# Optimization experiments

Measured on AMD Instinct MI355X. Metric: run time of the kernel, lower is better.

## Reference

```python
import jax, jax.numpy as jnp
import numpy as np

N_HEADS = 16
ALIBI_BIAS_MAX = 8


def _alibi_bias(n_heads, seq_len):
    # MPT build_alibi_bias: bias[h, j] = -(seq_len-1-j) * slope_h, arranged [1,H,1,S]
    pos = jnp.arange(1 - seq_len, 1, dtype=jnp.float32).reshape(1, 1, 1, seq_len)
    m = jnp.arange(1, n_heads + 1, dtype=jnp.float32) * (ALIBI_BIAS_MAX / n_heads)
    slopes = (1.0 / jnp.exp2(m)).reshape(1, n_heads, 1, 1)
    return pos * slopes  # [1,H,1,S]


def setup_inputs() -> dict:
    key = jax.random.key(0)
    k1, k2, k3 = jax.random.split(key, 3)
    B, S, D = 1, 2048, 2048
    x = jax.random.normal(k1, (B, S, D), dtype=jnp.float32)
    # Wqkv: Linear(D, 3D, bias=False); out_proj: Linear(D, D, bias=False)
    w_qkv = jax.random.normal(k2, (3 * D, D), dtype=jnp.float32) * (1.0 / np.sqrt(D))
    w_out = jax.random.normal(k3, (D, D), dtype=jnp.float32) * (1.0 / np.sqrt(D))
    return {"x": x, "w_qkv": w_qkv, "w_out": w_out}


def reference(x, w_qkv, w_out):
    B, S, D = x.shape
    H = N_HEADS
    d = D // H
    qkv = x @ w_qkv.T                              # [B,S,3D]
    q, k, v = jnp.split(qkv, 3, axis=-1)
    q = q.reshape(B, S, H, d).transpose(0, 2, 1, 3)  # [B,H,S,d]
    k = k.reshape(B, S, H, d).transpose(0, 2, 1, 3)
    v = v.reshape(B, S, H, d).transpose(0, 2, 1, 3)
    scale = 1.0 / np.sqrt(d)
    scores = jnp.einsum('bhqd,bhkd->bhqk', q, k) * scale  # [B,H,S,S]
    scores = scores + _alibi_bias(H, S)
    min_val = jnp.finfo(scores.dtype).min
    causal = jnp.tril(jnp.ones((S, S), dtype=bool))
    scores = jnp.where(causal[None, None, :, :], scores, min_val)
    probs = jax.nn.softmax(scores.astype(jnp.float32), axis=-1).astype(q.dtype)
    out = jnp.einsum('bhqk,bhkd->bhqd', probs, v)  # [B,H,S,d]
    out = out.transpose(0, 2, 1, 3).reshape(B, S, D)
    return out @ w_out.T
```

## Files before the change

### kernel.cpp

```cpp
#include <hip/hip_runtime.h>

typedef __bf16 bf16;
typedef __bf16 bf16x8 __attribute__((ext_vector_type(8)));
typedef __bf16 bf16x4 __attribute__((ext_vector_type(4)));
typedef float f32x4 __attribute__((ext_vector_type(4)));

#if __has_builtin(__builtin_amdgcn_exp2f)
#define EXP2(x) __builtin_amdgcn_exp2f(x)
#else
#define EXP2(x) exp2f(x)
#endif

__device__ __forceinline__ void gload_lds16(const void* g, void* l) {
  __builtin_amdgcn_global_load_lds(
      (const __attribute__((address_space(1))) void*)g,
      (__attribute__((address_space(3))) void*)l, 16, 0, 0);
}

__global__ __launch_bounds__(256) void cast_all(const float* __restrict__ x,
                                                const float* __restrict__ wqkv,
                                                const float* __restrict__ wout,
                                                bf16* __restrict__ x_bf,
                                                bf16* __restrict__ wqkv_bf,
                                                bf16* __restrict__ wout_bf) {
  const int b = blockIdx.x;
  const float* src;
  bf16* dst;
  int i;
  if (b < 4096) {
    src = x; dst = x_bf; i = b * 1024 + threadIdx.x * 4;
  } else if (b < 16384) {
    src = wqkv; dst = wqkv_bf; i = (b - 4096) * 1024 + threadIdx.x * 4;
  } else {
    src = wout; dst = wout_bf; i = (b - 16384) * 1024 + threadIdx.x * 4;
  }
  float4 v = *(const float4*)(src + i);
  bf16x4 o = {(bf16)v.x, (bf16)v.y, (bf16)v.z, (bf16)v.w};
  *(bf16x4*)(dst + i) = o;
}

__global__ __launch_bounds__(256) void gemm1_qkv(const bf16* __restrict__ A,
                                                 const bf16* __restrict__ B,
                                                 bf16* __restrict__ qb,
                                                 bf16* __restrict__ kb,
                                                 bf16* __restrict__ vt) {
  constexpr int K = 2048;
  __shared__ bf16 As[128 * 32];
  __shared__ bf16 Bs[128 * 32];
  const int t = threadIdx.x;
  const int w = t >> 6, l = t & 63;
  const int lr = l & 15, lg = l >> 4;
  const int nwg = 768;
  int lin = blockIdx.y * 48 + blockIdx.x;
  lin = (lin & 7) * (nwg >> 3) + (lin >> 3);
  const int bn = lin % 48;
  const int bm = lin / 48;
  const int wr = w >> 1, wc = w & 1;

  f32x4 acc[4][4] = {};
  const int row0 = t >> 2;
  const int cc0 = (t & 3) * 8;

  for (int k0 = 0; k0 < K; k0 += 32) {
#pragma unroll
    for (int r = 0; r < 2; ++r) {
      const int row = r * 64 + row0;
      gload_lds16(A + (size_t)(bm * 128 + row) * K + k0 + cc0,
                  (char*)As + (r * 256 + w * 64) * 16);
      gload_lds16(B + (size_t)(bn * 128 + row) * K + k0 + cc0,
                  (char*)Bs + (r * 256 + w * 64) * 16);
    }
    __syncthreads();
    bf16x8 af[4], bfr[4];
#pragma unroll
    for (int i = 0; i < 4; ++i) {
      af[i] = *(const bf16x8*)((const char*)As + (wr * 64 + i * 16 + lr) * 64 + lg * 16);
      bfr[i] = *(const bf16x8*)((const char*)Bs + (wc * 64 + i * 16 + lr) * 64 + lg * 16);
    }
#pragma unroll
    for (int mi = 0; mi < 4; ++mi)
#pragma unroll
      for (int ni = 0; ni < 4; ++ni)
        acc[mi][ni] = __builtin_amdgcn_mfma_f32_16x16x32_bf16(af[mi], bfr[ni],
                                                              acc[mi][ni], 0, 0, 0);
    __syncthreads();
  }

  const int mb = bm * 128 + wr * 64 + lg * 4;
  const int nb = bn * 128 + wc * 64 + lr;
  if (bn * 128 < 4096) {
    bf16* dst = (bn * 128 < 2048) ? qb : kb;
#pragma unroll
    for (int mi = 0; mi < 4; ++mi) {
      const int mg = mb + mi * 16;
#pragma unroll
      for (int ni = 0; ni < 4; ++ni) {
        const int ng = (nb + ni * 16) & 2047;
#pragma unroll
        for (int rr = 0; rr < 4; ++rr)
          dst[(size_t)(mg + rr) * 2048 + ng] = (bf16)acc[mi][ni][rr];
      }
    }
  } else {
#pragma unroll
    for (int mi = 0; mi < 4; ++mi) {
      const int mg = mb + mi * 16;
#pragma unroll
      for (int ni = 0; ni < 4; ++ni) {
        const int dc = nb + ni * 16 - 4096;
        bf16x4 pk = {(bf16)acc[mi][ni][0], (bf16)acc[mi][ni][1],
                     (bf16)acc[mi][ni][2], (bf16)acc[mi][ni][3]};
        *(bf16x4*)(vt + (size_t)dc * 2048 + mg) = pk;
      }
    }
  }
}

__global__ __launch_bounds__(256) void gemm2_64x128(const bf16* __restrict__ A,
                                                    const bf16* __restrict__ B,
                                                    float* __restrict__ Cf) {
  constexpr int K = 2048, N = 2048;
  __shared__ bf16 As[64 * 32];
  __shared__ bf16 Bs[128 * 32];
  const int t = threadIdx.x;
  const int w = t >> 6, l = t & 63;
  const int lr = l & 15, lg = l >> 4;
  int lin = blockIdx.y * 16 + blockIdx.x;
  lin = (lin & 7) * 64 + (lin >> 3);
  const int bn = lin % 16;
  const int bm = lin / 16;

  f32x4 acc[4][2] = {};

  for (int k0 = 0; k0 < K; k0 += 32) {
    {
      const int row = t >> 2;
      gload_lds16(A + (size_t)(bm * 64 + row) * K + k0 + (t & 3) * 8,
                  (char*)As + (w * 64) * 16);
    }
#pragma unroll
    for (int r = 0; r < 2; ++r) {
      const int c = r * 256 + t;
      const int row = c >> 2;
      gload_lds16(B + (size_t)(bn * 128 + row) * K + k0 + (c & 3) * 8,
                  (char*)Bs + (r * 256 + w * 64) * 16);
    }
    __syncthreads();
    bf16x8 af[4], bfr[2];
#pragma unroll
    for (int i = 0; i < 4; ++i)
      af[i] = *(const bf16x8*)((const char*)As + (i * 16 + lr) * 64 + lg * 16);
#pragma unroll
    for (int i = 0; i < 2; ++i)
      bfr[i] = *(const bf16x8*)((const char*)Bs + (w * 32 + i * 16 + lr) * 64 + lg * 16);
#pragma unroll
    for (int mi = 0; mi < 4; ++mi)
#pragma unroll
      for (int ni = 0; ni < 2; ++ni)
        acc[mi][ni] = __builtin_amdgcn_mfma_f32_16x16x32_bf16(af[mi], bfr[ni],
                                                              acc[mi][ni], 0, 0, 0);
    __syncthreads();
  }

  const int mb = bm * 64 + lg * 4;
  const int nb = bn * 128 + w * 32 + lr;
#pragma unroll
  for (int mi = 0; mi < 4; ++mi) {
    const int mg = mb + mi * 16;
#pragma unroll
    for (int ni = 0; ni < 2; ++ni) {
      const int ng = nb + ni * 16;
#pragma unroll
      for (int rr = 0; rr < 4; ++rr)
        Cf[(size_t)(mg + rr) * N + ng] = acc[mi][ni][rr];
    }
  }
}

__global__ __launch_bounds__(256) void attn_kernel(const bf16* __restrict__ qb,
                                                   const bf16* __restrict__ kb,
                                                   const bf16* __restrict__ vt,
                                                   bf16* __restrict__ out) {
  constexpr int S = 2048, D = 2048;
  __shared__ bf16 Ks[2][64 * 128];
  __shared__ bf16 Vs[2][128 * 64];
  __shared__ bf16 Ps[4][16 * 64];
  const int t = threadIdx.x;
  const int w = t >> 6, l = t & 63;
  const int lr = l & 15, lg = l >> 4;
  const int b = blockIdx.x;
  const int h = b & 15;
  const int qt = (b < 256) ? (31 - (b >> 4)) : ((b - 256) >> 4);
  const int q0 = qt * 64;
  const float slope2 = exp2f(-0.5f * (float)(h + 1)) * 1.4426950408889634f;
  const float scale2 = 0.08838834764831845f * 1.4426950408889634f;
  const int W = (int)(44.4f / slope2);
  const int s0 = (q0 > W) ? ((q0 - W) >> 6) : 0;

  bf16x8 qf[4];
  {
    const bf16* qrow = qb + (size_t)(q0 + w * 16 + lr) * D + h * 128 + lg * 8;
#pragma unroll
    for (int kk = 0; kk < 4; ++kk) qf[kk] = *(const bf16x8*)(qrow + kk * 32);
  }

  f32x4 ob[8] = {};
  float mrow[4] = {-1e30f, -1e30f, -1e30f, -1e30f};
  float lrow[4] = {0.f, 0.f, 0.f, 0.f};

  const int nt = qt + 1;

  auto stage = [&](int kv0, int bb) {
#pragma unroll
    for (int r = 0; r < 4; ++r) {
      {
        const int krow = r * 16 + (t >> 4);
        const int kcc = t & 15;
        gload_lds16(kb + (size_t)(kv0 + krow) * D + h * 128 + ((kcc ^ (krow & 7)) * 8),
                    (char*)Ks[bb] + (r * 256 + w * 64) * 16);
      }
      {
        const int vrow = r * 32 + (t >> 3);
        const int vcc = t & 7;
        gload_lds16(vt + (size_t)(h * 128 + vrow) * S + kv0 + ((vcc ^ (vrow & 7)) * 8),
                    (char*)Vs[bb] + (r * 256 + w * 64) * 16);
      }
    }
  };

  stage(s0 << 6, 0);
  int cur = 0;
  for (int tile = s0; tile < nt; ++tile) {
    __syncthreads();
    if (tile + 1 < nt) stage((tile + 1) << 6, cur ^ 1);
    const int kv0 = tile << 6;

    f32x4 sc[4] = {};
#pragma unroll
    for (int jb = 0; jb < 4; ++jb) {
      const int row = jb * 16 + lr;
#pragma unroll
      for (int kk = 0; kk < 4; ++kk) {
        const int byte = row * 256 + ((kk * 64 + lg * 16) ^ ((row & 7) << 4));
        bf16x8 kf = *(const bf16x8*)((const char*)Ks[cur] + byte);
        sc[jb] = __builtin_amdgcn_mfma_f32_16x16x32_bf16(qf[kk], kf, sc[jb], 0, 0, 0);
      }
    }

    float bias[4];
#pragma unroll
    for (int jb = 0; jb < 4; ++jb)
      bias[jb] = slope2 * (float)(kv0 + jb * 16 + lr - (S - 1));
    const bool diag = (tile == nt - 1);
    float xv[4][4], m2r[4];
#pragma unroll
    for (int rr = 0; rr < 4; ++rr) {
#pragma unroll
      for (int jb = 0; jb < 4; ++jb) {
        float v = fmaf(sc[jb][rr], scale2, bias[jb]);
        if (diag && (jb * 16 + lr > w * 16 + lg * 4 + rr)) v = -1e30f;
        xv[rr][jb] = v;
      }
      float m2 = fmaxf(fmaxf(xv[rr][0], xv[rr][1]), fmaxf(xv[rr][2], xv[rr][3]));
      m2 = fmaxf(m2, __shfl_xor(m2, 1));
      m2 = fmaxf(m2, __shfl_xor(m2, 2));
      m2 = fmaxf(m2, __shfl_xor(m2, 4));
      m2 = fmaxf(m2, __shfl_xor(m2, 8));
      m2r[rr] = m2;
    }
    float need = fmaxf(fmaxf(m2r[0] - mrow[0], m2r[1] - mrow[1]),
                       fmaxf(m2r[2] - mrow[2], m2r[3] - mrow[3]));
    if (!__all(need <= 8.0f)) {
#pragma unroll
      for (int rr = 0; rr < 4; ++rr) {
        const float mnew = fmaxf(mrow[rr], m2r[rr]);
        const float cf = EXP2(mrow[rr] - mnew);
        lrow[rr] *= cf;
        mrow[rr] = mnew;
#pragma unroll
        for (int db = 0; db < 8; ++db) ob[db][rr] *= cf;
      }
    }
    char* pbase = (char*)Ps[w];
#pragma unroll
    for (int rr = 0; rr < 4; ++rr) {
      const int prow = lg * 4 + rr;
      const int sw = (prow & 7) << 4;
      float ps = 0.f;
#pragma unroll
      for (int jb = 0; jb < 4; ++jb) {
        const float p = EXP2(xv[rr][jb] - mrow[rr]);
        *(bf16*)(pbase + ((prow * 128 + jb * 32 + lr * 2) ^ sw)) = (bf16)p;
        ps += p;
      }
      lrow[rr] += ps;
    }

    bf16x8 pf[2];
#pragma unroll
    for (int s = 0; s < 2; ++s)
      pf[s] = *(const bf16x8*)(pbase + ((lr * 128 + s * 64 + lg * 16) ^ ((lr & 7) << 4)));
#pragma unroll
    for (int db = 0; db < 8; ++db) {
      const int vrow = db * 16 + lr;
#pragma unroll
      for (int s = 0; s < 2; ++s) {
        const int byte = vrow * 128 + ((s * 64 + lg * 16) ^ ((vrow & 7) << 4));
        bf16x8 vf = *(const bf16x8*)((const char*)Vs[cur] + byte);
        ob[db] = __builtin_amdgcn_mfma_f32_16x16x32_bf16(pf[s], vf, ob[db], 0, 0, 0);
      }
    }
    cur ^= 1;
  }

#pragma unroll
  for (int rr = 0; rr < 4; ++rr) {
    float ls = lrow[rr];
    ls += __shfl_xor(ls, 1);
    ls += __shfl_xor(ls, 2);
    ls += __shfl_xor(ls, 4);
    ls += __shfl_xor(ls, 8);
    const float inv = 1.0f / ls;
    const int mg = q0 + w * 16 + lg * 4 + rr;
#pragma unroll
    for (int db = 0; db < 8; ++db)
      out[(size_t)mg * D + h * 128 + db * 16 + lr] = (bf16)(ob[db][rr] * inv);
  }
}

extern "C" void kernel_launch(void* const* d_in, const int* in_sizes, int n_in,
                              void* d_out, int out_size, void* d_ws, size_t ws_size,
                              hipStream_t stream) {
  (void)in_sizes; (void)n_in; (void)out_size; (void)ws_size;
  const float* x = (const float*)d_in[0];
  const float* wqkv = (const float*)d_in[1];
  const float* wout = (const float*)d_in[2];
  float* out = (float*)d_out;

  bf16* x_bf = (bf16*)d_ws;
  bf16* wqkv_bf = x_bf + (size_t)2048 * 2048;
  bf16* wout_bf = wqkv_bf + (size_t)6144 * 2048;
  bf16* qb = wout_bf + (size_t)2048 * 2048;
  bf16* kb = qb + (size_t)2048 * 2048;
  bf16* vt = kb + (size_t)2048 * 2048;
  bf16* attn = wqkv_bf;

  cast_all<<<20480, 256, 0, stream>>>(x, wqkv, wout, x_bf, wqkv_bf, wout_bf);
  gemm1_qkv<<<dim3(48, 16), 256, 0, stream>>>(x_bf, wqkv_bf, qb, kb, vt);
  attn_kernel<<<512, 256, 0, stream>>>(qb, kb, vt, attn);
  gemm2_64x128<<<dim3(16, 32), 256, 0, stream>>>(attn, wout_bf, out);
}
```

Measured before the change: 179.0 us.

## Split long causal attention tiles across two blocks with a merge kernel

The 256 heaviest query tiles (the upper half of the sequence) now have their KV range split between two blocks. Each block writes an unnormalized fp32 partial output plus its row max and sum to workspace, and a new merge kernel combines the pairs with the log-sum-exp rescale. The remaining tiles run unsplit as before. This is meant to even out load across the grid and give more parallelism, at the cost of an extra launch and fp32 partial-output traffic. It also raises wave priority around the MFMA sections with s_setprio.

```diff
diff --git a/kernel.cpp b/kernel.cpp
--- a/kernel.cpp
+++ b/kernel.cpp
@@ -180,7 +180,9 @@
 __global__ __launch_bounds__(256) void attn_kernel(const bf16* __restrict__ qb,
                                                    const bf16* __restrict__ kb,
                                                    const bf16* __restrict__ vt,
-                                                   bf16* __restrict__ out) {
+                                                   bf16* __restrict__ out,
+                                                   float* __restrict__ partO,
+                                                   float* __restrict__ ml) {
   constexpr int S = 2048, D = 2048;
   __shared__ bf16 Ks[2][64 * 128];
   __shared__ bf16 Vs[2][128 * 64];
@@ -189,13 +191,39 @@
   const int w = t >> 6, l = t & 63;
   const int lr = l & 15, lg = l >> 4;
   const int b = blockIdx.x;
-  const int h = b & 15;
-  const int qt = (b < 256) ? (31 - (b >> 4)) : ((b - 256) >> 4);
+
+  int h, qt, start, end, jobhalf;
+  bool split;
+  if (b < 512) {
+    split = true;
+    int j, sh;
+    if (b < 256) { j = b; sh = 0; } else { j = 511 - b; sh = 1; }
+    h = j & 15;
+    qt = 31 - (j >> 4);
+    jobhalf = j * 2 + sh;
+    const float sl2 = exp2f(-0.5f * (float)(h + 1)) * 1.4426950408889634f;
+    const int W = (int)(44.4f / sl2);
+    const int q0i = qt * 64;
+    const int s0 = (q0i > W) ? ((q0i - W) >> 6) : 0;
+    const int len = qt + 1 - s0;
+    const int l1 = (len + 1) >> 1;
+    start = sh ? s0 + l1 : s0;
+    end = sh ? qt + 1 : s0 + l1;
+  } else {
+    split = false;
+    const int i = b - 512;
+    h = i & 15;
+    qt = i >> 4;
+    jobhalf = 0;
+    const float sl2 = exp2f(-0.5f * (float)(h + 1)) * 1.4426950408889634f;
+    const int W = (int)(44.4f / sl2);
+    const int q0i = qt * 64;
+    start = (q0i > W) ? ((q0i - W) >> 6) : 0;
+    end = qt + 1;
+  }
   const int q0 = qt * 64;
   const float slope2 = exp2f(-0.5f * (float)(h + 1)) * 1.4426950408889634f;
   const float scale2 = 0.08838834764831845f * 1.4426950408889634f;
-  const int W = (int)(44.4f / slope2);
-  const int s0 = (q0 > W) ? ((q0 - W) >> 6) : 0;
 
   bf16x8 qf[4];
   {
@@ -207,8 +235,6 @@
   f32x4 ob[8] = {};
   float mrow[4] = {-1e30f, -1e30f, -1e30f, -1e30f};
   float lrow[4] = {0.f, 0.f, 0.f, 0.f};
-
-  const int nt = qt + 1;
 
   auto stage = [&](int kv0, int bb) {
 #pragma unroll
@@ -228,14 +254,15 @@
     }
   };
 
-  stage(s0 << 6, 0);
+  if (start < end) stage(start << 6, 0);
   int cur = 0;
-  for (int tile = s0; tile < nt; ++tile) {
+  for (int tile = start; tile < end; ++tile) {
     __syncthreads();
-    if (tile + 1 < nt) stage((tile + 1) << 6, cur ^ 1);
+    if (tile + 1 < end) stage((tile + 1) << 6, cur ^ 1);
     const int kv0 = tile << 6;
 
     f32x4 sc[4] = {};
+    __builtin_amdgcn_s_setprio(1);
 #pragma unroll
     for (int jb = 0; jb < 4; ++jb) {
       const int row = jb * 16 + lr;
@@ -246,12 +273,13 @@
         sc[jb] = __builtin_amdgcn_mfma_f32_16x16x32_bf16(qf[kk], kf, sc[jb], 0, 0, 0);
       }
     }
+    __builtin_amdgcn_s_setprio(0);
 
     float bias[4];
 #pragma unroll
     for (int jb = 0; jb < 4; ++jb)
       bias[jb] = slope2 * (float)(kv0 + jb * 16 + lr - (S - 1));
-    const bool diag = (tile == nt - 1);
+    const bool diag = (tile == qt);
     float xv[4][4], m2r[4];
 #pragma unroll
     for (int rr = 0; rr < 4; ++rr) {
@@ -300,6 +328,7 @@
 #pragma unroll
     for (int s = 0; s < 2; ++s)
       pf[s] = *(const bf16x8*)(pbase + ((lr * 128 + s * 64 + lg * 16) ^ ((lr & 7) << 4)));
+    __builtin_amdgcn_s_setprio(1);
 #pragma unroll
     for (int db = 0; db < 8; ++db) {
       const int vrow = db * 16 + lr;
@@ -310,21 +339,69 @@
         ob[db] = __builtin_amdgcn_mfma_f32_16x16x32_bf16(pf[s], vf, ob[db], 0, 0, 0);
       }
     }
+    __builtin_amdgcn_s_setprio(0);
     cur ^= 1;
   }
 
-#pragma unroll
-  for (int rr = 0; rr < 4; ++rr) {
-    float ls = lrow[rr];
-    ls += __shfl_xor(ls, 1);
-    ls += __shfl_xor(ls, 2);
-    ls += __shfl_xor(ls, 4);
-    ls += __shfl_xor(ls, 8);
-    const float inv = 1.0f / ls;
-    const int mg = q0 + w * 16 + lg * 4 + rr;
-#pragma unroll
-    for (int db = 0; db < 8; ++db)
-      out[(size_t)mg * D + h * 128 + db * 16 + lr] = (bf16)(ob[db][rr] * inv);
+  if (!split) {
+#pragma unroll
+    for (int rr = 0; rr < 4; ++rr) {
+      float ls = lrow[rr];
+      ls += __shfl_xor(ls, 1);
+      ls += __shfl_xor(ls, 2);
+      ls += __shfl_xor(ls, 4);
+      ls += __shfl_xor(ls, 8);
+      const float inv = 1.0f / ls;
+      const int mg = q0 + w * 16 + lg * 4 + rr;
+#pragma unroll
+      for (int db = 0; db < 8; ++db)
+        out[(size_t)mg * D + h * 128 + db * 16 + lr] = (bf16)(ob[db][rr] * inv);
+    }
+  } else {
+    float* po = partO + (size_t)jobhalf * 8192;
+#pragma unroll
+    for (int rr = 0; rr < 4; ++rr) {
+      float ls = lrow[rr];
+      ls += __shfl_xor(ls, 1);
+      ls += __shfl_xor(ls, 2);
+      ls += __shfl_xor(ls, 4);
+      ls += __shfl_xor(ls, 8);
+      const int row = w * 16 + lg * 4 + rr;
+#pragma unroll
+      for (int db = 0; db < 8; ++db)
+        po[row * 128 + db * 16 + lr] = ob[db][rr];
+      if (lr == 0) {
+        ml[jobhalf * 128 + row] = mrow[rr];
+        ml[jobhalf * 128 + 64 + row] = ls;
+      }
+    }
+  }
+}
+
+__global__ __launch_bounds__(256) void attn_merge(const float* __restrict__ partO,
+                                                  const float* __restrict__ ml,
+                                                  bf16* __restrict__ out) {
+  const int j = blockIdx.x;
+  const int t = threadIdx.x;
+  const int h = j & 15, qt = 31 - (j >> 4);
+  const int q0 = qt * 64;
+  const int row = t >> 2;
+  const int c0 = (t & 3) * 32;
+  const float m1 = ml[(2 * j) * 128 + row], l1 = ml[(2 * j) * 128 + 64 + row];
+  const float m2 = ml[(2 * j + 1) * 128 + row], l2 = ml[(2 * j + 1) * 128 + 64 + row];
+  const float M = fmaxf(m1, m2);
+  const float c1 = EXP2(m1 - M), c2 = EXP2(m2 - M);
+  const float inv = 1.0f / (c1 * l1 + c2 * l2);
+  const float* p1 = partO + (size_t)(2 * j) * 8192 + row * 128 + c0;
+  const float* p2 = partO + (size_t)(2 * j + 1) * 8192 + row * 128 + c0;
+  bf16* o = out + (size_t)(q0 + row) * 2048 + h * 128 + c0;
+#pragma unroll
+  for (int k = 0; k < 32; k += 4) {
+    f32x4 a = *(const f32x4*)(p1 + k);
+    f32x4 bb = *(const f32x4*)(p2 + k);
+    f32x4 r = (a * c1 + bb * c2) * inv;
+    bf16x4 o4 = {(bf16)r[0], (bf16)r[1], (bf16)r[2], (bf16)r[3]};
+    *(bf16x4*)(o + k) = o4;
   }
 }
 
@@ -344,9 +421,12 @@
   bf16* kb = qb + (size_t)2048 * 2048;
   bf16* vt = kb + (size_t)2048 * 2048;
   bf16* attn = wqkv_bf;
+  float* partO = (float*)(wqkv_bf + (size_t)2048 * 2048);
+  float* ml = (float*)x_bf;
 
   cast_all<<<20480, 256, 0, stream>>>(x, wqkv, wout, x_bf, wqkv_bf, wout_bf);
   gemm1_qkv<<<dim3(48, 16), 256, 0, stream>>>(x_bf, wqkv_bf, qb, kb, vt);
-  attn_kernel<<<512, 256, 0, stream>>>(qb, kb, vt, attn);
+  attn_kernel<<<768, 256, 0, stream>>>(qb, kb, vt, attn, partO, ml);
+  attn_merge<<<256, 256, 0, stream>>>(partO, ml, attn);
   gemm2_64x128<<<dim3(16, 32), 256, 0, stream>>>(attn, wout_bf, out);
 }
```

After: 169.9 us. -5.1%, faster.

## Split long attention query tiles across KV pieces and merge partials

Applied to the files above, without the earlier changes.

Query tiles 16-31 are split into four KV-range pieces and tiles 8-15 into two. This raises the attention grid from 512 to 1408 blocks and evens out per-block work, which the ALiBi window and causal mask had left skewed. Each split block writes its unnormalized partial output plus row max and sum into dead workspace regions. A new merge kernel then combines the partials with log-sum-exp weights. MFMA sections are also wrapped in s_setprio. The cost is an extra kernel launch and extra global traffic for the partials.

```diff
diff --git a/kernel.cpp b/kernel.cpp
--- a/kernel.cpp
+++ b/kernel.cpp
@@ -180,7 +180,10 @@
 __global__ __launch_bounds__(256) void attn_kernel(const bf16* __restrict__ qb,
                                                    const bf16* __restrict__ kb,
                                                    const bf16* __restrict__ vt,
-                                                   bf16* __restrict__ out) {
+                                                   bf16* __restrict__ out,
+                                                   bf16* __restrict__ pA,
+                                                   bf16* __restrict__ pB,
+                                                   float* __restrict__ ml) {
   constexpr int S = 2048, D = 2048;
   __shared__ bf16 Ks[2][64 * 128];
   __shared__ bf16 Vs[2][128 * 64];
@@ -189,13 +192,27 @@
   const int w = t >> 6, l = t & 63;
   const int lr = l & 15, lg = l >> 4;
   const int b = blockIdx.x;
-  const int h = b & 15;
-  const int qt = (b < 256) ? (31 - (b >> 4)) : ((b - 256) >> 4);
+
+  int h, qt, piece, ns;
+  if (b < 1024) {
+    const int j = b >> 2;
+    h = j & 15; qt = 16 + (j >> 4); piece = b & 3; ns = 4;
+  } else if (b < 1280) {
+    const int j = (b - 1024) >> 1;
+    h = j & 15; qt = 8 + (j >> 4); piece = (b - 1024) & 1; ns = 2;
+  } else {
+    const int i = b - 1280;
+    h = i & 15; qt = i >> 4; piece = 0; ns = 1;
+  }
+  const bool split = (ns > 1);
   const int q0 = qt * 64;
   const float slope2 = exp2f(-0.5f * (float)(h + 1)) * 1.4426950408889634f;
   const float scale2 = 0.08838834764831845f * 1.4426950408889634f;
   const int W = (int)(44.4f / slope2);
   const int s0 = (q0 > W) ? ((q0 - W) >> 6) : 0;
+  const int len = qt + 1 - s0;
+  const int start = s0 + (len * piece) / ns;
+  const int end = s0 + (len * (piece + 1)) / ns;
 
   bf16x8 qf[4];
   {
@@ -207,8 +224,6 @@
   f32x4 ob[8] = {};
   float mrow[4] = {-1e30f, -1e30f, -1e30f, -1e30f};
   float lrow[4] = {0.f, 0.f, 0.f, 0.f};
-
-  const int nt = qt + 1;
 
   auto stage = [&](int kv0, int bb) {
 #pragma unroll
@@ -228,14 +243,15 @@
     }
   };
 
-  stage(s0 << 6, 0);
+  if (start < end) stage(start << 6, 0);
   int cur = 0;
-  for (int tile = s0; tile < nt; ++tile) {
+  for (int tile = start; tile < end; ++tile) {
     __syncthreads();
-    if (tile + 1 < nt) stage((tile + 1) << 6, cur ^ 1);
+    if (tile + 1 < end) stage((tile + 1) << 6, cur ^ 1);
     const int kv0 = tile << 6;
 
     f32x4 sc[4] = {};
+    __builtin_amdgcn_s_setprio(1);
 #pragma unroll
     for (int jb = 0; jb < 4; ++jb) {
       const int row = jb * 16 + lr;
@@ -246,12 +262,13 @@
         sc[jb] = __builtin_amdgcn_mfma_f32_16x16x32_bf16(qf[kk], kf, sc[jb], 0, 0, 0);
       }
     }
+    __builtin_amdgcn_s_setprio(0);
 
     float bias[4];
 #pragma unroll
     for (int jb = 0; jb < 4; ++jb)
       bias[jb] = slope2 * (float)(kv0 + jb * 16 + lr - (S - 1));
-    const bool diag = (tile == nt - 1);
+    const bool diag = (tile == qt);
     float xv[4][4], m2r[4];
 #pragma unroll
     for (int rr = 0; rr < 4; ++rr) {
@@ -300,6 +317,7 @@
 #pragma unroll
     for (int s = 0; s < 2; ++s)
       pf[s] = *(const bf16x8*)(pbase + ((lr * 128 + s * 64 + lg * 16) ^ ((lr & 7) << 4)));
+    __builtin_amdgcn_s_setprio(1);
 #pragma unroll
     for (int db = 0; db < 8; ++db) {
       const int vrow = db * 16 + lr;
@@ -310,21 +328,92 @@
         ob[db] = __builtin_amdgcn_mfma_f32_16x16x32_bf16(pf[s], vf, ob[db], 0, 0, 0);
       }
     }
+    __builtin_amdgcn_s_setprio(0);
     cur ^= 1;
   }
 
-#pragma unroll
-  for (int rr = 0; rr < 4; ++rr) {
-    float ls = lrow[rr];
-    ls += __shfl_xor(ls, 1);
-    ls += __shfl_xor(ls, 2);
-    ls += __shfl_xor(ls, 4);
-    ls += __shfl_xor(ls, 8);
-    const float inv = 1.0f / ls;
-    const int mg = q0 + w * 16 + lg * 4 + rr;
-#pragma unroll
-    for (int db = 0; db < 8; ++db)
-      out[(size_t)mg * D + h * 128 + db * 16 + lr] = (bf16)(ob[db][rr] * inv);
+  if (!split) {
+#pragma unroll
+    for (int rr = 0; rr < 4; ++rr) {
+      float ls = lrow[rr];
+      ls += __shfl_xor(ls, 1);
+      ls += __shfl_xor(ls, 2);
+      ls += __shfl_xor(ls, 4);
+      ls += __shfl_xor(ls, 8);
+      const float inv = 1.0f / ls;
+      const int mg = q0 + w * 16 + lg * 4 + rr;
+#pragma unroll
+      for (int db = 0; db < 8; ++db)
+        out[(size_t)mg * D + h * 128 + db * 16 + lr] = (bf16)(ob[db][rr] * inv);
+    }
+  } else {
+    bf16* po = (b < 1024) ? pA + (size_t)b * 8192 : pB + (size_t)(b - 1024) * 8192;
+#pragma unroll
+    for (int rr = 0; rr < 4; ++rr) {
+      float ls = lrow[rr];
+      ls += __shfl_xor(ls, 1);
+      ls += __shfl_xor(ls, 2);
+      ls += __shfl_xor(ls, 4);
+      ls += __shfl_xor(ls, 8);
+      const int row = w * 16 + lg * 4 + rr;
+#pragma unroll
+      for (int db = 0; db < 8; ++db)
+        po[row * 128 + db * 16 + lr] = (bf16)ob[db][rr];
+      if (lr == 0) {
+        ml[b * 128 + row] = mrow[rr];
+        ml[b * 128 + 64 + row] = ls;
+      }
+    }
+  }
+}
+
+__global__ __launch_bounds__(256) void attn_merge(const bf16* __restrict__ pA,
+                                                  const bf16* __restrict__ pB,
+                                                  const float* __restrict__ ml,
+                                                  bf16* __restrict__ out) {
+  const int j = blockIdx.x;
+  const int t = threadIdx.x;
+  int ns, c0, h, qt;
+  if (j < 256) {
+    ns = 4; c0 = 4 * j; h = j & 15; qt = 16 + (j >> 4);
+  } else {
+    const int j2 = j - 256;
+    ns = 2; c0 = 1024 + 2 * j2; h = j2 & 15; qt = 8 + (j2 >> 4);
+  }
+  const int q0 = qt * 64;
+  const int row = t >> 2;
+  const int col0 = (t & 3) * 32;
+
+  float m[4], lv[4];
+  float M = -1e30f;
+  for (int i = 0; i < ns; ++i) {
+    m[i] = ml[(c0 + i) * 128 + row];
+    lv[i] = ml[(c0 + i) * 128 + 64 + row];
+    M = fmaxf(M, m[i]);
+  }
+  float wsum = 0.f, wgt[4];
+  for (int i = 0; i < ns; ++i) {
+    wgt[i] = EXP2(m[i] - M);
+    wsum += wgt[i] * lv[i];
+  }
+  const float inv = 1.0f / wsum;
+
+  float accv[32] = {};
+  for (int i = 0; i < ns; ++i) {
+    const int c = c0 + i;
+    const bf16* po = (c < 1024) ? pA + (size_t)c * 8192 : pB + (size_t)(c - 1024) * 8192;
+    const bf16* pr = po + row * 128 + col0;
+    const float wi = wgt[i];
+#pragma unroll
+    for (int k = 0; k < 32; ++k) accv[k] += wi * (float)pr[k];
+  }
+  bf16* o = out + (size_t)(q0 + row) * 2048 + h * 128 + col0;
+#pragma unroll
+  for (int k = 0; k < 4; ++k) {
+    bf16x8 o8;
+#pragma unroll
+    for (int e = 0; e < 8; ++e) o8[e] = (bf16)(accv[k * 8 + e] * inv);
+    *(bf16x8*)(o + k * 8) = o8;
   }
 }
 
@@ -344,9 +433,13 @@
   bf16* kb = qb + (size_t)2048 * 2048;
   bf16* vt = kb + (size_t)2048 * 2048;
   bf16* attn = wqkv_bf;
+  bf16* pA = wqkv_bf + (size_t)2048 * 2048;
+  bf16* pB = x_bf;
+  float* ml = (float*)((char*)d_ws + (size_t)4 * 1024 * 1024);
 
   cast_all<<<20480, 256, 0, stream>>>(x, wqkv, wout, x_bf, wqkv_bf, wout_bf);
   gemm1_qkv<<<dim3(48, 16), 256, 0, stream>>>(x_bf, wqkv_bf, qb, kb, vt);
-  attn_kernel<<<512, 256, 0, stream>>>(qb, kb, vt, attn);
+  attn_kernel<<<1408, 256, 0, stream>>>(qb, kb, vt, attn, pA, pB, ml);
+  attn_merge<<<384, 256, 0, stream>>>(pA, pB, ml, attn);
   gemm2_64x128<<<dim3(16, 32), 256, 0, stream>>>(attn, wout_bf, out);
 }
```

Measured after the change: 171.1 us. 1.05x faster.
